# Kernel optimization log

Measured on AMD Instinct MI355X. Metric: run time of the kernel, lower is better.

Reference implementation:

```python
import jax, jax.numpy as jnp
import numpy as np

BS = 8  # JPEG block size

LUMINANCE_QUANTIZATION_TABLE = np.array((
    (16, 11, 10, 16, 24, 40, 51, 61),
    (12, 12, 14, 19, 26, 58, 60, 55),
    (14, 13, 16, 24, 40, 57, 69, 56),
    (14, 17, 22, 29, 51, 87, 80, 62),
    (18, 22, 37, 56, 68, 109, 103, 77),
    (24, 36, 55, 64, 81, 104, 113, 92),
    (49, 64, 78, 87, 103, 121, 120, 101),
    (72, 92, 95, 98, 112, 100, 103, 99)), dtype=np.float64)
Q_TABLE = (LUMINANCE_QUANTIZATION_TABLE / 100.0).astype(np.float32)  # matches process_Q_table


def _dct_matrix(N):
    # Orthonormal DCT-II matrix C[k, n] = f_k * cos(pi*(2n+1)*k/(2N)),
    # identical math to grid_factors * cos(DCT_freq_grid * (2*DCT_arange + 1)) in the torch code
    n = np.arange(N)[None, :]
    k = np.arange(N)[:, None]
    C = np.cos(np.pi * (2 * n + 1) * k / (2.0 * N))
    f = np.full((N, 1), np.sqrt(2.0 / N))
    f[0, 0] = 1.0 / np.sqrt(N)
    return (f * C).astype(np.float32)

_DCT_MAT = _dct_matrix(BS)


def setup_inputs() -> dict:
    key = jax.random.key(0)
    k1, k2 = jax.random.split(key)
    image = jax.random.uniform(k1, (16, 1, 1024, 1024), dtype=jnp.float32) * 255.0
    quality_factor = jax.random.uniform(k2, (16,), dtype=jnp.float32, minval=10.0, maxval=90.0)
    return {"image": image, "quality_factor": quality_factor}


def reference(image, quality_factor):
    B, _, H, W = image.shape
    hb, wb = H // BS, W // BS
    # Image_2_Blocks: [B,1,H,W] -> [B, 8, 8, hb, wb]
    blocks = image.reshape(B, hb, BS, wb, BS).transpose(0, 2, 4, 1, 3)
    blocks = blocks - 128.0
    C = jnp.asarray(_DCT_MAT)
    # Blocks_DCT: orthonormal 2D DCT-II over the two 8-dims (axes 1 and 2)
    out = jnp.einsum('kn,bnmhw->bkmhw', C, blocks)
    out = jnp.einsum('lm,bkmhw->bklhw', C, out)
    # Set_QF factor: 5000/QF if QF<50 else 200-2*QF
    factor = jnp.where(quality_factor < 50.0, 5000.0 / quality_factor, 200.0 - 2.0 * quality_factor)
    factor = factor.reshape(B, 1, 1, 1, 1)
    Q = jnp.asarray(Q_TABLE).reshape(1, BS, BS, 1, 1)
    out = out / (factor * Q)
    # downsample_and_quantize=False -> no rounding
    return out.reshape(B, BS * BS, hb, wb)
```

## Files before the change

### kernel.cpp

```cpp
#include <hip/hip_runtime.h>
#include <hip/hip_bf16.h>


#define BS 8
#define HPIX 1024
#define WPIX 1024
#define HB (HPIX / BS)
#define WB (WPIX / BS)
#define BATCH 16

constexpr float DCT[8][8] = {
  { 0.35355339059327373f,  0.35355339059327373f,  0.35355339059327373f,  0.35355339059327373f,
    0.35355339059327373f,  0.35355339059327373f,  0.35355339059327373f,  0.35355339059327373f },
  { 0.49039264020161522f,  0.41573480615127262f,  0.27778511650980114f,  0.09754516100806413f,
   -0.09754516100806413f, -0.27778511650980114f, -0.41573480615127262f, -0.49039264020161522f },
  { 0.46193976625564337f,  0.19134171618254492f, -0.19134171618254492f, -0.46193976625564337f,
   -0.46193976625564337f, -0.19134171618254492f,  0.19134171618254492f,  0.46193976625564337f },
  { 0.41573480615127262f, -0.09754516100806413f, -0.49039264020161522f, -0.27778511650980114f,
    0.27778511650980114f,  0.49039264020161522f,  0.09754516100806413f, -0.41573480615127262f },
  { 0.35355339059327373f, -0.35355339059327373f, -0.35355339059327373f,  0.35355339059327373f,
    0.35355339059327373f, -0.35355339059327373f, -0.35355339059327373f,  0.35355339059327373f },
  { 0.27778511650980114f, -0.49039264020161522f,  0.09754516100806413f,  0.41573480615127262f,
   -0.41573480615127262f, -0.09754516100806413f,  0.49039264020161522f, -0.27778511650980114f },
  { 0.19134171618254492f, -0.46193976625564337f,  0.46193976625564337f, -0.19134171618254492f,
   -0.19134171618254492f,  0.46193976625564337f, -0.46193976625564337f,  0.19134171618254492f },
  { 0.09754516100806413f, -0.27778511650980114f,  0.41573480615127262f, -0.49039264020161522f,
    0.49039264020161522f, -0.41573480615127262f,  0.27778511650980114f, -0.09754516100806413f },
};

constexpr float INVQ[8][8] = {
  { 6.25f,              9.09090909090909f,  10.0f,              6.25f,
    4.16666666666667f,  2.5f,               1.96078431372549f,  1.63934426229508f },
  { 8.33333333333333f,  8.33333333333333f,  7.14285714285714f,  5.26315789473684f,
    3.84615384615385f,  1.72413793103448f,  1.66666666666667f,  1.81818181818182f },
  { 7.14285714285714f,  7.69230769230769f,  6.25f,              4.16666666666667f,
    2.5f,               1.75438596491228f,  1.44927536231884f,  1.78571428571429f },
  { 7.14285714285714f,  5.88235294117647f,  4.54545454545455f,  3.44827586206897f,
    1.96078431372549f,  1.14942528735632f,  1.25f,              1.61290322580645f },
  { 5.55555555555556f,  4.54545454545455f,  2.70270270270270f,  1.78571428571429f,
    1.47058823529412f,  0.91743119266055f,  0.970873786407767f, 1.29870129870130f },
  { 4.16666666666667f,  2.77777777777778f,  1.81818181818182f,  1.5625f,
    1.23456790123457f,  0.961538461538462f, 0.884955752212389f, 1.08695652173913f },
  { 2.04081632653061f,  1.5625f,            1.28205128205128f,  1.14942528735632f,
    0.970873786407767f, 0.826446280991736f, 0.833333333333333f, 0.990099009900990f },
  { 1.38888888888889f,  1.08695652173913f,  1.05263157894737f,  1.02040816326531f,
    0.892857142857143f, 1.0f,               0.970873786407767f, 1.01010101010101f },
};

__global__ __launch_bounds__(256, 4) void jpeg_dct_q_kernel(
    const float* __restrict__ img,
    const float* __restrict__ qf,
    float* __restrict__ out)
{
    __shared__ float lds[4][2][8][64];

    const int t = threadIdx.x;
    const int lane = t & 63;
    const int wv = t >> 6;
    const int g = blockIdx.x;
    const int b = g >> 6;
    const int h0 = (g & 63) << 1;
    const int hsub = wv >> 1;
    const int wbase = (wv & 1) << 6;
    const int w = wbase + lane;
    const int h = h0 + hsub;

    const float* rowbase = img + ((size_t)b << 20) + (size_t)(h * BS) * WPIX + (size_t)(w * BS);

    float4 va[8], vb[8];
#pragma unroll
    for (int n = 0; n < 8; ++n) {
        const float4* p = reinterpret_cast<const float4*>(rowbase + n * WPIX);
        va[n] = p[0];
        vb[n] = p[1];
    }

    float r[8][8];
#pragma unroll
    for (int n = 0; n < 8; ++n) {
        r[n][0] = va[n].x - 128.0f; r[n][1] = va[n].y - 128.0f;
        r[n][2] = va[n].z - 128.0f; r[n][3] = va[n].w - 128.0f;
        r[n][4] = vb[n].x - 128.0f; r[n][5] = vb[n].y - 128.0f;
        r[n][6] = vb[n].z - 128.0f; r[n][7] = vb[n].w - 128.0f;
    }

    const float q = qf[b];
    const float factor = (q < 50.0f) ? (5000.0f / q) : (200.0f - 2.0f * q);
    const float rf = 1.0f / factor;

    const int row0 = lane >> 4;
    const int chunk = lane & 15;
    const size_t obatch = (size_t)b << 20;

#pragma unroll
    for (int k = 0; k < 8; ++k) {
        const int buf = k & 1;

        float tk[8];
#pragma unroll
        for (int m = 0; m < 8; ++m)
            tk[m] = 0.0f;
#pragma unroll
        for (int n = 0; n < 8; ++n) {
            const float cf = DCT[k][n];
#pragma unroll
            for (int m = 0; m < 8; ++m)
                tk[m] = fmaf(cf, r[n][m], tk[m]);
        }

#pragma unroll
        for (int l = 0; l < 8; ++l) {
            float s = 0.0f;
#pragma unroll
            for (int m = 0; m < 8; ++m)
                s = fmaf(DCT[l][m], tk[m], s);
            lds[wv][buf][l][lane] = s * rf * INVQ[k][l];
        }

#pragma unroll
        for (int it = 0; it < 2; ++it) {
            const int row = row0 + 4 * it;
            float4 v = *reinterpret_cast<const float4*>(&lds[wv][buf][row][4 * chunk]);
            float* dst = out + obatch + (size_t)(k * 8 + row) * (HB * WB)
                             + (size_t)h * WB + wbase + 4 * chunk;
            *reinterpret_cast<float4*>(dst) = v;
        }
    }
}

extern "C" void kernel_launch(void* const* d_in, const int* in_sizes, int n_in,
                              void* d_out, int out_size, void* d_ws, size_t ws_size,
                              hipStream_t stream) {
    const float* img = (const float*)d_in[0];
    const float* qf  = (const float*)d_in[1];
    float* out = (float*)d_out;

    const int grid = BATCH * (HB / 2);
    const int block = 256;

    jpeg_dct_q_kernel<<<grid, block, 0, stream>>>(img, qf, out);
}
```

Measured before the change: 111.3 us.

## Process two block rows per thread with loads hoisted, fold -128 shift into DC

Each thread now loads two 8x8 blocks up front (issuing all 32 float4 loads before any compute) and processes them in sequence, with the grid halved and launch bounds lowered to 2 blocks per CU. The -128 level shift is removed from every pixel and applied once as a constant subtracted from the k=0 row-DCT term. The aim is more memory-level parallelism per thread and fewer ALU ops, at the cost of higher register pressure and fewer resident waves. There is also a risk of a WAR hazard on the per-wave LDS buffer between the two blocks, since there is no barrier.

```diff
diff --git a/kernel.cpp b/kernel.cpp
--- a/kernel.cpp
+++ b/kernel.cpp
@@ -47,51 +47,14 @@
     0.892857142857143f, 1.0f,               0.970873786407767f, 1.01010101010101f },
 };
 
-__global__ __launch_bounds__(256, 4) void jpeg_dct_q_kernel(
-    const float* __restrict__ img,
-    const float* __restrict__ qf,
-    float* __restrict__ out)
+#define K0_SHIFT 362.03867196751236f
+
+__device__ __forceinline__ void process_block(
+    const float4 v0[8], const float4 v1[8],
+    float rf, int lane, int row0, int chunk,
+    float (&ldsw)[2][8][64],
+    float* __restrict__ dstbase)
 {
-    __shared__ float lds[4][2][8][64];
-
-    const int t = threadIdx.x;
-    const int lane = t & 63;
-    const int wv = t >> 6;
-    const int g = blockIdx.x;
-    const int b = g >> 6;
-    const int h0 = (g & 63) << 1;
-    const int hsub = wv >> 1;
-    const int wbase = (wv & 1) << 6;
-    const int w = wbase + lane;
-    const int h = h0 + hsub;
-
-    const float* rowbase = img + ((size_t)b << 20) + (size_t)(h * BS) * WPIX + (size_t)(w * BS);
-
-    float4 va[8], vb[8];
-#pragma unroll
-    for (int n = 0; n < 8; ++n) {
-        const float4* p = reinterpret_cast<const float4*>(rowbase + n * WPIX);
-        va[n] = p[0];
-        vb[n] = p[1];
-    }
-
-    float r[8][8];
-#pragma unroll
-    for (int n = 0; n < 8; ++n) {
-        r[n][0] = va[n].x - 128.0f; r[n][1] = va[n].y - 128.0f;
-        r[n][2] = va[n].z - 128.0f; r[n][3] = va[n].w - 128.0f;
-        r[n][4] = vb[n].x - 128.0f; r[n][5] = vb[n].y - 128.0f;
-        r[n][6] = vb[n].z - 128.0f; r[n][7] = vb[n].w - 128.0f;
-    }
-
-    const float q = qf[b];
-    const float factor = (q < 50.0f) ? (5000.0f / q) : (200.0f - 2.0f * q);
-    const float rf = 1.0f / factor;
-
-    const int row0 = lane >> 4;
-    const int chunk = lane & 15;
-    const size_t obatch = (size_t)b << 20;
-
 #pragma unroll
     for (int k = 0; k < 8; ++k) {
         const int buf = k & 1;
@@ -103,9 +66,19 @@
 #pragma unroll
         for (int n = 0; n < 8; ++n) {
             const float cf = DCT[k][n];
+            tk[0] = fmaf(cf, v0[n].x, tk[0]);
+            tk[1] = fmaf(cf, v0[n].y, tk[1]);
+            tk[2] = fmaf(cf, v0[n].z, tk[2]);
+            tk[3] = fmaf(cf, v0[n].w, tk[3]);
+            tk[4] = fmaf(cf, v1[n].x, tk[4]);
+            tk[5] = fmaf(cf, v1[n].y, tk[5]);
+            tk[6] = fmaf(cf, v1[n].z, tk[6]);
+            tk[7] = fmaf(cf, v1[n].w, tk[7]);
+        }
+        if (k == 0) {
 #pragma unroll
             for (int m = 0; m < 8; ++m)
-                tk[m] = fmaf(cf, r[n][m], tk[m]);
+                tk[m] -= K0_SHIFT;
         }
 
 #pragma unroll
@@ -114,18 +87,69 @@
 #pragma unroll
             for (int m = 0; m < 8; ++m)
                 s = fmaf(DCT[l][m], tk[m], s);
-            lds[wv][buf][l][lane] = s * rf * INVQ[k][l];
+            ldsw[buf][l][lane] = s * rf * INVQ[k][l];
         }
 
 #pragma unroll
         for (int it = 0; it < 2; ++it) {
             const int row = row0 + 4 * it;
-            float4 v = *reinterpret_cast<const float4*>(&lds[wv][buf][row][4 * chunk]);
-            float* dst = out + obatch + (size_t)(k * 8 + row) * (HB * WB)
-                             + (size_t)h * WB + wbase + 4 * chunk;
+            float4 v = *reinterpret_cast<const float4*>(&ldsw[buf][row][4 * chunk]);
+            float* dst = dstbase + (size_t)(k * 8 + row) * (HB * WB) + 4 * chunk;
             *reinterpret_cast<float4*>(dst) = v;
         }
     }
+}
+
+__global__ __launch_bounds__(256, 2) void jpeg_dct_q_kernel(
+    const float* __restrict__ img,
+    const float* __restrict__ qf,
+    float* __restrict__ out)
+{
+    __shared__ float lds[4][2][8][64];
+
+    const int t = threadIdx.x;
+    const int lane = t & 63;
+    const int wv = t >> 6;
+    const int g = blockIdx.x;
+    const int b = g >> 5;
+    const int h0 = (g & 31) << 2;
+    const int hsub = wv >> 1;
+    const int wbase = (wv & 1) << 6;
+    const int w = wbase + lane;
+    const int hA = h0 + hsub;
+    const int hB = h0 + 2 + hsub;
+
+    const float* baseA = img + ((size_t)b << 20) + (size_t)(hA * BS) * WPIX + (size_t)(w * BS);
+    const float* baseB = img + ((size_t)b << 20) + (size_t)(hB * BS) * WPIX + (size_t)(w * BS);
+
+    float4 a0[8], a1[8], b0[8], b1[8];
+#pragma unroll
+    for (int n = 0; n < 8; ++n) {
+        const float4* p = reinterpret_cast<const float4*>(baseA + n * WPIX);
+        a0[n] = p[0];
+        a1[n] = p[1];
+    }
+#pragma unroll
+    for (int n = 0; n < 8; ++n) {
+        const float4* p = reinterpret_cast<const float4*>(baseB + n * WPIX);
+        b0[n] = p[0];
+        b1[n] = p[1];
+    }
+    asm volatile("" ::: "memory");
+
+    const float q = qf[b];
+    const float factor = (q < 50.0f) ? (5000.0f / q) : (200.0f - 2.0f * q);
+    const float rf = 1.0f / factor;
+
+    const int row0 = lane >> 4;
+    const int chunk = lane & 15;
+    const size_t obatch = (size_t)b << 20;
+
+    float* dstA = out + obatch + (size_t)hA * WB + wbase;
+    float* dstB = out + obatch + (size_t)hB * WB + wbase;
+
+    process_block(a0, a1, rf, lane, row0, chunk, lds[wv], dstA);
+    process_block(b0, b1, rf, lane, row0, chunk, lds[wv], dstB);
 }
 
 extern "C" void kernel_launch(void* const* d_in, const int* in_sizes, int n_in,
@@ -135,7 +159,7 @@
     const float* qf  = (const float*)d_in[1];
     float* out = (float*)d_out;
 
-    const int grid = BATCH * (HB / 2);
+    const int grid = BATCH * (HB / 4);
     const int block = 256;
 
     jpeg_dct_q_kernel<<<grid, block, 0, stream>>>(img, qf, out);
```

Measured after the change: 116.1 us. 1.04x slower.
